# Kernel tuning notes

Hardware: AMD Instinct MI355X
Metric: run time of the kernel (lower is better)

The kernel has to match this reference:

```python
import jax, jax.numpy as jnp
import numpy as np

B, C, H, W, G = 4, 256, 64, 64, 4
K = 9  # 3x3 kernel


def _conv1x1(x, w, b):
    return jnp.einsum('bchw,oc->bohw', x, w) + b[None, :, None, None]


def _deform_conv(V, offset, mask, weight, groups):
    # torchvision modulated deform_conv2d, stride=1, pad=1, dil=1, no bias.
    Bs, Cc, Hh, Ww = V.shape
    Cg = Cc // groups
    # offset layout: [B, og, K, 2(y,x), H, W]
    off = offset.reshape(Bs, groups, K, 2, Hh, Ww)
    ky, kx = jnp.meshgrid(jnp.arange(3), jnp.arange(3), indexing='ij')
    ky = ky.reshape(K).astype(offset.dtype)
    kx = kx.reshape(K).astype(offset.dtype)
    hh = jnp.arange(Hh, dtype=offset.dtype)
    ww = jnp.arange(Ww, dtype=offset.dtype)
    # sampling positions [B, G, K, H, W]
    py = off[:, :, :, 0] + (hh[:, None] - 1.0)[None, None, None] + ky[None, None, :, None, None]
    px = off[:, :, :, 1] + (ww[None, :] - 1.0)[None, None, None] + kx[None, None, :, None, None]
    y0f = jnp.floor(py)
    x0f = jnp.floor(px)
    fy = py - y0f
    fx = px - x0f
    y0 = y0f.astype(jnp.int32)
    x0 = x0f.astype(jnp.int32)
    Vg = V.reshape(Bs, groups, Cg, Hh * Ww)

    def gather(yi, xi, wgt):
        valid = (yi >= 0) & (yi < Hh) & (xi >= 0) & (xi < Ww)
        idx = (jnp.clip(yi, 0, Hh - 1) * Ww + jnp.clip(xi, 0, Ww - 1)).reshape(Bs, groups, 1, K * Hh * Ww)
        vals = jnp.take_along_axis(Vg, jnp.broadcast_to(idx, (Bs, groups, Cg, K * Hh * Ww)), axis=3)
        vals = vals.reshape(Bs, groups, Cg, K, Hh, Ww)
        return vals * (wgt * valid.astype(wgt.dtype))[:, :, None]

    sampled = (gather(y0, x0, (1.0 - fy) * (1.0 - fx))
               + gather(y0, x0 + 1, (1.0 - fy) * fx)
               + gather(y0 + 1, x0, fy * (1.0 - fx))
               + gather(y0 + 1, x0 + 1, fy * fx))  # [B, G, Cg, K, H, W]
    m = mask.reshape(Bs, groups, K, Hh, Ww)
    wk = weight.reshape(groups, Cc // groups, Cg, K)
    out = jnp.einsum('bgikhw,bgkhw,goik->bgohw', sampled, m, wk)
    return out.reshape(Bs, Cc, Hh, Ww)


def setup_inputs() -> dict:
    key = jax.random.key(0)
    ks = jax.random.split(key, 12)
    inp = {
        'rife_feat': jax.random.normal(ks[0], (B, C, H, W), jnp.float32),
        'd0': jax.random.normal(ks[1], (B, C, H, W), jnp.float32),
        'd1': jax.random.normal(ks[2], (B, C, H, W), jnp.float32),
        'wq': jax.random.normal(ks[3], (C, C), jnp.float32) * (1.0 / np.sqrt(C)),
        'bq': jax.random.normal(ks[4], (C,), jnp.float32) * 0.01,
        'wk': jax.random.normal(ks[5], (C, C), jnp.float32) * (1.0 / np.sqrt(C)),
        'bk': jax.random.normal(ks[6], (C,), jnp.float32) * 0.01,
        'wv': jax.random.normal(ks[7], (C, C), jnp.float32) * (1.0 / np.sqrt(C)),
        'bv': jax.random.normal(ks[8], (C,), jnp.float32) * 0.01,
        'w_off': jax.random.normal(ks[9], (27 * G, 2 * C, 3, 3), jnp.float32) * 0.02,
        'b_off': jnp.zeros((27 * G,), jnp.float32),
        'dcn_w': jax.random.normal(ks[10], (C, C // G, 3, 3), jnp.float32) * 0.05,
        'gamma': jnp.ones((1,), jnp.float32),
    }
    return inp


def reference(rife_feat, d0, d1, wq, bq, wk, bk, wv, bv, w_off, b_off, dcn_w, gamma):
    Qs = jnp.concatenate([rife_feat, rife_feat], axis=0)  # [2B, C, H, W]
    Ds = jnp.concatenate([d0, d1], axis=0)
    Q = _conv1x1(Qs, wq, bq)
    Kf = _conv1x1(Ds, wk, bk)
    V = _conv1x1(Ds, wv, bv)
    comb = jnp.concatenate([Q, Kf], axis=1)  # [2B, 2C, H, W]
    out = jax.lax.conv_general_dilated(comb, w_off, (1, 1), [(1, 1), (1, 1)],
                                       dimension_numbers=('NCHW', 'OIHW', 'NCHW'))
    out = out + b_off[None, :, None, None]  # [2B, 27G, H, W]
    n = out.shape[1] // 3
    o1, o2, mlog = out[:, :n], out[:, n:2 * n], out[:, 2 * n:]
    offset = jnp.concatenate([o1, o2], axis=1)  # [2B, 18G, H, W]
    mask = jax.nn.sigmoid(mlog)
    aligned = _deform_conv(V, offset, mask, dcn_w, G)
    a0, a1 = aligned[:B], aligned[B:]
    fused = rife_feat + gamma * (a0 + a1)
    return fused, offset[:B], offset[B:]
```

## Files before the change

kernel.cpp:

```cpp
#include <hip/hip_runtime.h>
#include <math.h>

#define HW   4096
#define CDIM 256

typedef float f32x4  __attribute__((ext_vector_type(4)));
typedef short short8 __attribute__((ext_vector_type(8)));

#define FUSED_SZ (4ULL*256*HW)
#define OFF_SZ   (4ULL*72*HW)

static __device__ __forceinline__ unsigned short f2b(float f) {
    unsigned u = __float_as_uint(f);
    unsigned r = (u + 0x7fffu + ((u >> 16) & 1u)) >> 16;
    return (unsigned short)r;
}
static __device__ __forceinline__ float b2f(short h) {
    return __uint_as_float(((unsigned)(unsigned short)h) << 16);
}
static __device__ __forceinline__ unsigned pk_bf16(float a, float b) {
    unsigned r;
    asm("v_cvt_pk_bf16_f32 %0, %1, %2" : "=v"(r) : "v"(a), "v"(b));
    return r;
}
union U8 { unsigned u[4]; short8 s; };

__global__ __launch_bounds__(256) void prep_all(
    const float* __restrict__ w_off, const float* __restrict__ dcn_w,
    const float* __restrict__ wq, const float* __restrict__ wk,
    const float* __restrict__ wv,
    unsigned short* __restrict__ wT2, unsigned short* __restrict__ dcnwT,
    unsigned short* __restrict__ wqkvT)
{
    const int bid = blockIdx.x;
    if (bid < 2304) {
        int idx = bid * 256 + threadIdx.x;
        int kk  = idx / (128 * 512);
        int rem = idx - kk * 128 * 512;
        int o = rem >> 9;
        int c = rem & 511;
        float v = (o < 108) ? w_off[((size_t)o * 512 + c) * 9 + kk] : 0.f;
        size_t flat = ((size_t)(kk * 16 + (c >> 5)) * 128 + o) * 32 + (c & 31);
        wT2[flat] = f2b(v);
    } else if (bid < 2880) {
        int idx = (bid - 2304) * 256 + threadIdx.x;
        if (idx < 9 * 256 * 64) {
            int k   = idx / (256 * 64);
            int rem = idx - k * 256 * 64;
            int og = rem >> 6;
            int i  = rem & 63;
            int g = og >> 6, ol = og & 63;
            size_t flat = ((size_t)((k * 4 + g) * 2 + (i >> 5)) * 64 + ol) * 32 + (i & 31);
            dcnwT[flat] = f2b(dcn_w[((size_t)og * 64 + i) * 9 + k]);
        }
    } else {
        int idx = (bid - 2880) * 256 + threadIdx.x;
        int o = idx >> 8;
        int c = idx & 255;
        float v = (o < 256) ? wq[(size_t)o * 256 + c]
                : (o < 512) ? wk[(size_t)(o - 256) * 256 + c]
                            : wv[(size_t)(o - 512) * 256 + c];
        wqkvT[idx] = f2b(v);
    }
}

__global__ __launch_bounds__(256) void xprep(
    const float* __restrict__ rife, const float* __restrict__ d0,
    const float* __restrict__ d1, unsigned short* __restrict__ xT)
{
    const int pix0 = blockIdx.x * 64;
    const int img  = blockIdx.y;
    const int t    = threadIdx.x;

    const float* src = (img < 4) ? rife + (size_t)img * CDIM * HW
                     : (img < 8) ? d0 + (size_t)(img - 4) * CDIM * HW
                                 : d1 + (size_t)(img - 8) * CDIM * HW;
    unsigned short* dst = xT + (size_t)img * 4096 * 256;

    __shared__ float tile[64][65];

    for (int c0 = 0; c0 < 256; c0 += 64) {
        #pragma unroll
        for (int r = 0; r < 16; ++r) {
            int idx = t + r * 256;
            int c = idx >> 6, pp = idx & 63;
            tile[c][pp] = src[(size_t)(c0 + c) * HW + pix0 + pp];
        }
        __syncthreads();
        const int pix = t >> 2, cq = t & 3;
        const int cb = cq * 16;
        uint4 p0, p1;
        p0.x = pk_bf16(tile[cb+0][pix],  tile[cb+1][pix]);
        p0.y = pk_bf16(tile[cb+2][pix],  tile[cb+3][pix]);
        p0.z = pk_bf16(tile[cb+4][pix],  tile[cb+5][pix]);
        p0.w = pk_bf16(tile[cb+6][pix],  tile[cb+7][pix]);
        p1.x = pk_bf16(tile[cb+8][pix],  tile[cb+9][pix]);
        p1.y = pk_bf16(tile[cb+10][pix], tile[cb+11][pix]);
        p1.z = pk_bf16(tile[cb+12][pix], tile[cb+13][pix]);
        p1.w = pk_bf16(tile[cb+14][pix], tile[cb+15][pix]);
        unsigned short* p = dst + (size_t)(pix0 + pix) * 256 + c0 + cb;
        *(uint4*)p = p0;
        *(uint4*)(p + 8) = p1;
        __syncthreads();
    }
}

__global__ __launch_bounds__(256) void qkv_mfma(
    const unsigned short* __restrict__ xT,
    const unsigned short* __restrict__ wqkvT,
    const float* __restrict__ bq, const float* __restrict__ bk,
    const float* __restrict__ bv,
    unsigned short* __restrict__ comb_t, unsigned short* __restrict__ vbuf_t)
{
    const int pix0 = blockIdx.x * 64;
    const int type = blockIdx.y;
    const int s    = blockIdx.z;
    const int t    = threadIdx.x;
    const int wvi  = t >> 6;
    const int lane = t & 63;
    const int q    = lane >> 4;
    const int rl   = lane & 15;

    const int img = (type == 0) ? (s & 3) : (4 + s);
    const short8* X = (const short8*)(xT + (size_t)img * 4096 * 256);
    const short8* W = (const short8*)(wqkvT + (size_t)(type * 256 + wvi * 64) * 256);
    const float* bias = (type == 0) ? bq : (type == 1) ? bk : bv;

    f32x4 acc[4][4];
    #pragma unroll
    for (int mf = 0; mf < 4; ++mf)
        #pragma unroll
        for (int nf = 0; nf < 4; ++nf)
            acc[mf][nf] = (f32x4){0.f, 0.f, 0.f, 0.f};

    #pragma unroll
    for (int c8 = 0; c8 < 32; c8 += 4) {
        short8 a[4], b[4];
        #pragma unroll
        for (int mf = 0; mf < 4; ++mf)
            a[mf] = W[(size_t)(mf * 16 + rl) * 32 + c8 + q];
        #pragma unroll
        for (int nf = 0; nf < 4; ++nf)
            b[nf] = X[(size_t)(pix0 + nf * 16 + rl) * 32 + c8 + q];
        #pragma unroll
        for (int mf = 0; mf < 4; ++mf)
            #pragma unroll
            for (int nf = 0; nf < 4; ++nf)
                acc[mf][nf] = __builtin_amdgcn_mfma_f32_16x16x32_bf16(a[mf], b[nf], acc[mf][nf], 0, 0, 0);
    }

    const int CH = (type < 2) ? 512 : 256;
    unsigned short* dst = (type < 2)
        ? comb_t + (size_t)s * 4096 * 512 + type * 256
        : vbuf_t + (size_t)s * 4096 * 256;
    #pragma unroll
    for (int mf = 0; mf < 4; ++mf) {
        const int o_loc = wvi * 64 + mf * 16 + q * 4;
        const float4 bz = *(const float4*)(bias + o_loc);
        #pragma unroll
        for (int nf = 0; nf < 4; ++nf) {
            const int pix = pix0 + nf * 16 + rl;
            uint2 pk;
            pk.x = pk_bf16(acc[mf][nf][0] + bz.x, acc[mf][nf][1] + bz.y);
            pk.y = pk_bf16(acc[mf][nf][2] + bz.z, acc[mf][nf][3] + bz.w);
            *(uint2*)(dst + (size_t)pix * CH + o_loc) = pk;
        }
    }
}

__global__ __launch_bounds__(256) void offconv_mfma(
    const unsigned short* __restrict__ comb_t,
    const unsigned short* __restrict__ wT2,
    const float* __restrict__ b_off,
    float* __restrict__ dout, float* __restrict__ mask_ws)
{
    const int bid = blockIdx.x;
    const int s = bid & 7;
    const int h = bid >> 3;
    const int t = threadIdx.x;
    const int lane = t & 63;
    const int wid  = t >> 6;
    const int q    = lane >> 4;
    const int rl   = lane & 15;

    __shared__ __align__(16) unsigned short tb[2][792 * 8];

    const short8* cbv = (const short8*)comb_t + (size_t)s * 4096 * 64;
    const short8* wv  = (const short8*)wT2;

    const int i1 = t + 256, i2 = t + 512, i3 = t + 768;

    auto sload = [&](int idx, int c8) -> short8 {
        int x = idx >> 2, cq = idx & 3;
        int ky = x / 66, xx = x - ky * 66;
        int hh = h + ky - 1, gx = xx - 1;
        short8 v = {0, 0, 0, 0, 0, 0, 0, 0};
        if (hh >= 0 && hh < 64 && gx >= 0 && gx < 64)
            v = cbv[(size_t)(hh * 64 + gx) * 64 + c8 + cq];
        return v;
    };
    auto swrite = [&](unsigned short* buf, int idx, short8 v) {
        int x = idx >> 2, cq = idx & 3;
        int qs = cq ^ ((x >> 1) & 3);
        *((short8*)buf + x * 4 + qs) = v;
    };

    f32x4 acc[2][4];
    #pragma unroll
    for (int ma = 0; ma < 2; ++ma)
        #pragma unroll
        for (int nf = 0; nf < 4; ++nf)
            acc[ma][nf] = (f32x4){0.f, 0.f, 0.f, 0.f};

    short8 r0 = sload(t, 0), r1 = sload(i1, 0), r2 = sload(i2, 0);
    short8 r3 = {0,0,0,0,0,0,0,0};
    if (i3 < 792) r3 = sload(i3, 0);
    swrite(tb[0], t, r0); swrite(tb[0], i1, r1); swrite(tb[0], i2, r2);
    if (i3 < 792) swrite(tb[0], i3, r3);
    __syncthreads();

    for (int sl = 0; sl < 16; ++sl) {
        const int c8 = sl * 4;
        if (sl < 15) {
            r0 = sload(t, c8 + 4); r1 = sload(i1, c8 + 4); r2 = sload(i2, c8 + 4);
            if (i3 < 792) r3 = sload(i3, c8 + 4);
        }
        short8 a[2][9];
        #pragma unroll
        for (int ma = 0; ma < 2; ++ma) {
            const int o = (wid * 2 + ma) * 16 + rl;
            #pragma unroll
            for (int kk = 0; kk < 9; ++kk)
                a[ma][kk] = wv[((size_t)(kk * 16 + sl) * 128 + o) * 4 + q];
        }
        const unsigned short* bufc = tb[sl & 1];
        #pragma unroll
        for (int kk = 0; kk < 9; ++kk) {
            const int ky = kk / 3, kx = kk % 3;
            #pragma unroll
            for (int nf = 0; nf < 4; ++nf) {
                const int xr = ky * 66 + nf * 16 + rl + kx;
                short8 b = *((const short8*)bufc + xr * 4 + (q ^ ((xr >> 1) & 3)));
                acc[0][nf] = __builtin_amdgcn_mfma_f32_16x16x32_bf16(a[0][kk], b, acc[0][nf], 0, 0, 0);
                acc[1][nf] = __builtin_amdgcn_mfma_f32_16x16x32_bf16(a[1][kk], b, acc[1][nf], 0, 0, 0);
            }
        }
        if (sl < 15) {
            unsigned short* bufn = tb[(sl + 1) & 1];
            swrite(bufn, t, r0); swrite(bufn, i1, r1); swrite(bufn, i2, r2);
            if (i3 < 792) swrite(bufn, i3, r3);
        }
        __syncthreads();
    }

    const size_t obase = FUSED_SZ + (s < 4 ? 0 : OFF_SZ) + (size_t)(s & 3) * 72 * HW + (size_t)h * 64;
    const size_t mbase = (size_t)s * 36 * HW + (size_t)h * 64;
    #pragma unroll
    for (int ma = 0; ma < 2; ++ma) {
        #pragma unroll
        for (int r = 0; r < 4; ++r) {
            const int o = (wid * 2 + ma) * 16 + q * 4 + r;
            if (o >= 108) continue;
            const float bz = b_off[o];
            #pragma unroll
            for (int nf = 0; nf < 4; ++nf) {
                const int w = nf * 16 + rl;
                float v = acc[ma][nf][r] + bz;
                if (o < 72)
                    dout[obase + (size_t)o * HW + w] = v;
                else
                    mask_ws[mbase + (size_t)(o - 72) * HW + w] = 1.f / (1.f + expf(-v));
            }
        }
    }
}

__global__ __launch_bounds__(256) void dcn_fuse_mfma(
    const float* __restrict__ rife, const unsigned short* __restrict__ dcnwT,
    const float* __restrict__ gamma,
    const unsigned short* __restrict__ vbuf_t, const float* __restrict__ mask_ws,
    float* __restrict__ dout)
{
    const int bid = blockIdx.x;
    const int c   = bid & 15;
    const int h   = bid >> 4;
    const int b   = c >> 2;
    const int g   = c & 3;
    const int t    = threadIdx.x;
    const int wv   = t >> 6;
    const int lane = t & 63;
    const int q    = lane >> 4;
    const int rl   = lane & 15;
    const int pix  = wv * 16 + rl;

    const short8* aT = (const short8*)dcnwT;

    f32x4 acc[4];
    #pragma unroll
    for (int ma = 0; ma < 4; ++ma) acc[ma] = (f32x4){0.f, 0.f, 0.f, 0.f};

    const size_t obA = FUSED_SZ + (size_t)b * 72 * HW + (size_t)(g * 18) * HW + (size_t)h * 64 + pix;
    const size_t obB = obA + OFF_SZ;
    const size_t mbA = (size_t)b * 36 * HW + (size_t)(g * 9) * HW + (size_t)h * 64 + pix;
    const size_t mbB = mbA + 4ULL * 36 * HW;

    const unsigned short* VbA = vbuf_t + (size_t)b * 4096 * 256 + g * 64 + q * 8;
    const unsigned short* VbB = VbA + 4ULL * 4096 * 256;

    auto bil = [&](float py, float px, float mv,
                   float& w00, float& w01, float& w10, float& w11,
                   size_t& o00, size_t& o01, size_t& o10, size_t& o11) {
        const float y0f = floorf(py), x0f = floorf(px);
        const float fy = py - y0f, fx = px - x0f;
        const int y0 = (int)y0f, x0 = (int)x0f;
        const bool vy0 = (y0 >= 0) && (y0 < 64);
        const bool vy1 = (y0 >= -1) && (y0 < 63);
        const bool vx0 = (x0 >= 0) && (x0 < 64);
        const bool vx1 = (x0 >= -1) && (x0 < 63);
        w00 = (1.f - fy) * (1.f - fx) * mv * (float)(vy0 && vx0);
        w01 = (1.f - fy) * fx        * mv * (float)(vy0 && vx1);
        w10 = fy * (1.f - fx)        * mv * (float)(vy1 && vx0);
        w11 = fy * fx                * mv * (float)(vy1 && vx1);
        const int yc0 = min(max(y0, 0), 63),     yc1 = min(max(y0 + 1, 0), 63);
        const int xc0 = min(max(x0, 0), 63),     xc1 = min(max(x0 + 1, 0), 63);
        o00 = (size_t)(yc0 * 64 + xc0) * 256;
        o01 = (size_t)(yc0 * 64 + xc1) * 256;
        o10 = (size_t)(yc1 * 64 + xc0) * 256;
        o11 = (size_t)(yc1 * 64 + xc1) * 256;
    };
    auto blend1 = [&](short8 c00, short8 c01, short8 c10, short8 c11,
                      float w00, float w01, float w10, float w11) -> short8 {
        U8 u;
        #pragma unroll
        for (int j = 0; j < 4; ++j) {
            const int ce = 2 * j, co = 2 * j + 1;
            float e0 = w00 * b2f(c00[ce]) + w01 * b2f(c01[ce])
                     + w10 * b2f(c10[ce]) + w11 * b2f(c11[ce]);
            float e1 = w00 * b2f(c00[co]) + w01 * b2f(c01[co])
                     + w10 * b2f(c10[co]) + w11 * b2f(c11[co]);
            u.u[j] = pk_bf16(e0, e1);
        }
        return u.s;
    };

    float cyA = dout[obA], cxA = dout[obA + HW], cmA = mask_ws[mbA];
    float cyB = dout[obB], cxB = dout[obB + HW], cmB = mask_ws[mbB];

    for (int k = 0; k < 9; ++k) {
        const int ky = k / 3, kx = k - ky * 3;

        float wA00, wA01, wA10, wA11, wB00, wB01, wB10, wB11;
        size_t oA00, oA01, oA10, oA11, oB00, oB01, oB10, oB11;
        bil(cyA + (float)(h - 1 + ky), cxA + (float)(pix - 1 + kx), cmA,
            wA00, wA01, wA10, wA11, oA00, oA01, oA10, oA11);
        bil(cyB + (float)(h - 1 + ky), cxB + (float)(pix - 1 + kx), cmB,
            wB00, wB01, wB10, wB11, oB00, oB01, oB10, oB11);

        float nyA = cyA, nxA = cxA, nmA = cmA;
        float nyB = cyB, nxB = cxB, nmB = cmB;
        if (k < 8) {
            nyA = dout[obA + (size_t)((k + 1) * 2) * HW];
            nxA = dout[obA + (size_t)((k + 1) * 2 + 1) * HW];
            nmA = mask_ws[mbA + (size_t)(k + 1) * HW];
            nyB = dout[obB + (size_t)((k + 1) * 2) * HW];
            nxB = dout[obB + (size_t)((k + 1) * 2 + 1) * HW];
            nmB = mask_ws[mbB + (size_t)(k + 1) * HW];
        }

        #pragma unroll
        for (int ks = 0; ks < 2; ++ks) {
            const int co = ks * 32;
            short8 af0 = aT[((size_t)((k * 4 + g) * 2 + ks) * 64 + 0 * 16 + rl) * 4 + q];
            short8 af1 = aT[((size_t)((k * 4 + g) * 2 + ks) * 64 + 1 * 16 + rl) * 4 + q];
            short8 af2 = aT[((size_t)((k * 4 + g) * 2 + ks) * 64 + 2 * 16 + rl) * 4 + q];
            short8 af3 = aT[((size_t)((k * 4 + g) * 2 + ks) * 64 + 3 * 16 + rl) * 4 + q];
            short8 A00 = *(const short8*)(VbA + oA00 + co);
            short8 A01 = *(const short8*)(VbA + oA01 + co);
            short8 A10 = *(const short8*)(VbA + oA10 + co);
            short8 A11 = *(const short8*)(VbA + oA11 + co);
            short8 B00 = *(const short8*)(VbB + oB00 + co);
            short8 B01 = *(const short8*)(VbB + oB01 + co);
            short8 B10 = *(const short8*)(VbB + oB10 + co);
            short8 B11 = *(const short8*)(VbB + oB11 + co);

            short8 bfA = blend1(A00, A01, A10, A11, wA00, wA01, wA10, wA11);
            acc[0] = __builtin_amdgcn_mfma_f32_16x16x32_bf16(af0, bfA, acc[0], 0, 0, 0);
            acc[1] = __builtin_amdgcn_mfma_f32_16x16x32_bf16(af1, bfA, acc[1], 0, 0, 0);
            acc[2] = __builtin_amdgcn_mfma_f32_16x16x32_bf16(af2, bfA, acc[2], 0, 0, 0);
            acc[3] = __builtin_amdgcn_mfma_f32_16x16x32_bf16(af3, bfA, acc[3], 0, 0, 0);
            short8 bfB = blend1(B00, B01, B10, B11, wB00, wB01, wB10, wB11);
            acc[0] = __builtin_amdgcn_mfma_f32_16x16x32_bf16(af0, bfB, acc[0], 0, 0, 0);
            acc[1] = __builtin_amdgcn_mfma_f32_16x16x32_bf16(af1, bfB, acc[1], 0, 0, 0);
            acc[2] = __builtin_amdgcn_mfma_f32_16x16x32_bf16(af2, bfB, acc[2], 0, 0, 0);
            acc[3] = __builtin_amdgcn_mfma_f32_16x16x32_bf16(af3, bfB, acc[3], 0, 0, 0);
        }

        cyA = nyA; cxA = nxA; cmA = nmA;
        cyB = nyB; cxB = nxB; cmB = nmB;
    }

    const float gm = gamma[0];
    #pragma unroll
    for (int ma = 0; ma < 4; ++ma) {
        #pragma unroll
        for (int r = 0; r < 4; ++r) {
            const int o = g * 64 + ma * 16 + q * 4 + r;
            const size_t addr = ((size_t)b * 256 + o) * HW + (size_t)h * 64 + pix;
            dout[addr] = rife[addr] + gm * acc[ma][r];
        }
    }
}

extern "C" void kernel_launch(void* const* d_in, const int* in_sizes, int n_in,
                              void* d_out, int out_size, void* d_ws, size_t ws_size,
                              hipStream_t stream)
{
    const float* rife  = (const float*)d_in[0];
    const float* d0    = (const float*)d_in[1];
    const float* d1    = (const float*)d_in[2];
    const float* wq    = (const float*)d_in[3];
    const float* bq    = (const float*)d_in[4];
    const float* wk    = (const float*)d_in[5];
    const float* bk    = (const float*)d_in[6];
    const float* wv    = (const float*)d_in[7];
    const float* bv    = (const float*)d_in[8];
    const float* w_off = (const float*)d_in[9];
    const float* b_off = (const float*)d_in[10];
    const float* dcnw  = (const float*)d_in[11];
    const float* gamma = (const float*)d_in[12];
    float* out = (float*)d_out;
    char* wsb  = (char*)d_ws;

    unsigned short* comb_t = (unsigned short*)(wsb);
    unsigned short* vbuf_t = (unsigned short*)(wsb + 33554432);
    float*          mws    = (float*)(wsb + 50331648);
    unsigned short* wT2    = (unsigned short*)(wsb + 55050240);
    unsigned short* dcnwT  = (unsigned short*)(wsb + 56229888);
    unsigned short* xT     = (unsigned short*)(wsb + 56524800);
    unsigned short* wqkvT  = (unsigned short*)(wsb + 81690624);

    prep_all<<<3648, 256, 0, stream>>>(w_off, dcnw, wq, wk, wv, wT2, dcnwT, wqkvT);
    xprep<<<dim3(64, 12), 256, 0, stream>>>(rife, d0, d1, xT);
    qkv_mfma<<<dim3(64, 3, 8), 256, 0, stream>>>(xT, wqkvT, bq, bk, bv, comb_t, vbuf_t);
    offconv_mfma<<<512, 256, 0, stream>>>(comb_t, wT2, b_off, out, mws);
    dcn_fuse_mfma<<<1024, 256, 0, stream>>>(rife, dcnwT, gamma, vbuf_t, mws, out);
}
```

Measured before the change: 220.0 us.

## Split DCN A/B halves across two wave groups with LDS reduction

The deformable-conv kernel now launches 512 threads per block. The first four waves process the batch-A (d0) samples and the second four process batch-B (d1), where before each thread handled both serially. Partial accumulators from the B half are reduced through a 16KB shared-memory buffer and a barrier before the fused output write. This doubles wave-level parallelism and halves the per-thread gather latency chain. The cost is the LDS traffic, the sync, and redundant weight-fragment loads in both halves.

```diff
diff --git a/kernel.cpp b/kernel.cpp
--- a/kernel.cpp
+++ b/kernel.cpp
@@ -275,7 +275,7 @@
     }
 }
 
-__global__ __launch_bounds__(256) void dcn_fuse_mfma(
+__global__ __launch_bounds__(512) void dcn_fuse_mfma(
     const float* __restrict__ rife, const unsigned short* __restrict__ dcnwT,
     const float* __restrict__ gamma,
     const unsigned short* __restrict__ vbuf_t, const float* __restrict__ mask_ws,
@@ -287,7 +287,9 @@
     const int b   = c >> 2;
     const int g   = c & 3;
     const int t    = threadIdx.x;
-    const int wv   = t >> 6;
+    const int wave = t >> 6;
+    const int sbi  = wave >> 2;
+    const int wv   = wave & 3;
     const int lane = t & 63;
     const int q    = lane >> 4;
     const int rl   = lane & 15;
@@ -295,17 +297,16 @@
 
     const short8* aT = (const short8*)dcnwT;
 
+    __shared__ __align__(16) float red[256 * 16];
+
     f32x4 acc[4];
     #pragma unroll
     for (int ma = 0; ma < 4; ++ma) acc[ma] = (f32x4){0.f, 0.f, 0.f, 0.f};
 
-    const size_t obA = FUSED_SZ + (size_t)b * 72 * HW + (size_t)(g * 18) * HW + (size_t)h * 64 + pix;
-    const size_t obB = obA + OFF_SZ;
-    const size_t mbA = (size_t)b * 36 * HW + (size_t)(g * 9) * HW + (size_t)h * 64 + pix;
-    const size_t mbB = mbA + 4ULL * 36 * HW;
-
-    const unsigned short* VbA = vbuf_t + (size_t)b * 4096 * 256 + g * 64 + q * 8;
-    const unsigned short* VbB = VbA + 4ULL * 4096 * 256;
+    const size_t ob = FUSED_SZ + (sbi ? OFF_SZ : 0)
+                    + (size_t)b * 72 * HW + (size_t)(g * 18) * HW + (size_t)h * 64 + pix;
+    const size_t mb = (size_t)(sbi * 4 + b) * 36 * HW + (size_t)(g * 9) * HW + (size_t)h * 64 + pix;
+    const unsigned short* Vb = vbuf_t + (size_t)(sbi * 4 + b) * 4096 * 256 + g * 64 + q * 8;
 
     auto bil = [&](float py, float px, float mv,
                    float& w00, float& w01, float& w10, float& w11,
@@ -343,28 +344,21 @@
         return u.s;
     };
 
-    float cyA = dout[obA], cxA = dout[obA + HW], cmA = mask_ws[mbA];
-    float cyB = dout[obB], cxB = dout[obB + HW], cmB = mask_ws[mbB];
+    float cy = dout[ob], cx = dout[ob + HW], cm = mask_ws[mb];
 
     for (int k = 0; k < 9; ++k) {
         const int ky = k / 3, kx = k - ky * 3;
 
-        float wA00, wA01, wA10, wA11, wB00, wB01, wB10, wB11;
-        size_t oA00, oA01, oA10, oA11, oB00, oB01, oB10, oB11;
-        bil(cyA + (float)(h - 1 + ky), cxA + (float)(pix - 1 + kx), cmA,
-            wA00, wA01, wA10, wA11, oA00, oA01, oA10, oA11);
-        bil(cyB + (float)(h - 1 + ky), cxB + (float)(pix - 1 + kx), cmB,
-            wB00, wB01, wB10, wB11, oB00, oB01, oB10, oB11);
-
-        float nyA = cyA, nxA = cxA, nmA = cmA;
-        float nyB = cyB, nxB = cxB, nmB = cmB;
+        float w00, w01, w10, w11;
+        size_t o00, o01, o10, o11;
+        bil(cy + (float)(h - 1 + ky), cx + (float)(pix - 1 + kx), cm,
+            w00, w01, w10, w11, o00, o01, o10, o11);
+
+        float ny = cy, nx = cx, nm = cm;
         if (k < 8) {
-            nyA = dout[obA + (size_t)((k + 1) * 2) * HW];
-            nxA = dout[obA + (size_t)((k + 1) * 2 + 1) * HW];
-            nmA = mask_ws[mbA + (size_t)(k + 1) * HW];
-            nyB = dout[obB + (size_t)((k + 1) * 2) * HW];
-            nxB = dout[obB + (size_t)((k + 1) * 2 + 1) * HW];
-            nmB = mask_ws[mbB + (size_t)(k + 1) * HW];
+            ny = dout[ob + (size_t)((k + 1) * 2) * HW];
+            nx = dout[ob + (size_t)((k + 1) * 2 + 1) * HW];
+            nm = mask_ws[mb + (size_t)(k + 1) * HW];
         }
 
         #pragma unroll
@@ -374,39 +368,40 @@
             short8 af1 = aT[((size_t)((k * 4 + g) * 2 + ks) * 64 + 1 * 16 + rl) * 4 + q];
             short8 af2 = aT[((size_t)((k * 4 + g) * 2 + ks) * 64 + 2 * 16 + rl) * 4 + q];
             short8 af3 = aT[((size_t)((k * 4 + g) * 2 + ks) * 64 + 3 * 16 + rl) * 4 + q];
-            short8 A00 = *(const short8*)(VbA + oA00 + co);
-            short8 A01 = *(const short8*)(VbA + oA01 + co);
-            short8 A10 = *(const short8*)(VbA + oA10 + co);
-            short8 A11 = *(const short8*)(VbA + oA11 + co);
-            short8 B00 = *(const short8*)(VbB + oB00 + co);
-            short8 B01 = *(const short8*)(VbB + oB01 + co);
-            short8 B10 = *(const short8*)(VbB + oB10 + co);
-            short8 B11 = *(const short8*)(VbB + oB11 + co);
-
-            short8 bfA = blend1(A00, A01, A10, A11, wA00, wA01, wA10, wA11);
-            acc[0] = __builtin_amdgcn_mfma_f32_16x16x32_bf16(af0, bfA, acc[0], 0, 0, 0);
-            acc[1] = __builtin_amdgcn_mfma_f32_16x16x32_bf16(af1, bfA, acc[1], 0, 0, 0);
-            acc[2] = __builtin_amdgcn_mfma_f32_16x16x32_bf16(af2, bfA, acc[2], 0, 0, 0);
-            acc[3] = __builtin_amdgcn_mfma_f32_16x16x32_bf16(af3, bfA, acc[3], 0, 0, 0);
-            short8 bfB = blend1(B00, B01, B10, B11, wB00, wB01, wB10, wB11);
-            acc[0] = __builtin_amdgcn_mfma_f32_16x16x32_bf16(af0, bfB, acc[0], 0, 0, 0);
-            acc[1] = __builtin_amdgcn_mfma_f32_16x16x32_bf16(af1, bfB, acc[1], 0, 0, 0);
-            acc[2] = __builtin_amdgcn_mfma_f32_16x16x32_bf16(af2, bfB, acc[2], 0, 0, 0);
-            acc[3] = __builtin_amdgcn_mfma_f32_16x16x32_bf16(af3, bfB, acc[3], 0, 0, 0);
-        }
-
-        cyA = nyA; cxA = nxA; cmA = nmA;
-        cyB = nyB; cxB = nxB; cmB = nmB;
-    }
-
-    const float gm = gamma[0];
-    #pragma unroll
-    for (int ma = 0; ma < 4; ++ma) {
-        #pragma unroll
-        for (int r = 0; r < 4; ++r) {
-            const int o = g * 64 + ma * 16 + q * 4 + r;
-            const size_t addr = ((size_t)b * 256 + o) * HW + (size_t)h * 64 + pix;
-            dout[addr] = rife[addr] + gm * acc[ma][r];
+            short8 C00 = *(const short8*)(Vb + o00 + co);
+            short8 C01 = *(const short8*)(Vb + o01 + co);
+            short8 C10 = *(const short8*)(Vb + o10 + co);
+            short8 C11 = *(const short8*)(Vb + o11 + co);
+
+            short8 bf = blend1(C00, C01, C10, C11, w00, w01, w10, w11);
+            acc[0] = __builtin_amdgcn_mfma_f32_16x16x32_bf16(af0, bf, acc[0], 0, 0, 0);
+            acc[1] = __builtin_amdgcn_mfma_f32_16x16x32_bf16(af1, bf, acc[1], 0, 0, 0);
+            acc[2] = __builtin_amdgcn_mfma_f32_16x16x32_bf16(af2, bf, acc[2], 0, 0, 0);
+            acc[3] = __builtin_amdgcn_mfma_f32_16x16x32_bf16(af3, bf, acc[3], 0, 0, 0);
+        }
+
+        cy = ny; cx = nx; cm = nm;
+    }
+
+    if (sbi == 1) {
+        float* dst = &red[(t - 256) * 16];
+        #pragma unroll
+        for (int ma = 0; ma < 4; ++ma)
+            *(f32x4*)(dst + ma * 4) = acc[ma];
+    }
+    __syncthreads();
+    if (sbi == 0) {
+        const float* src = &red[t * 16];
+        const float gm = gamma[0];
+        #pragma unroll
+        for (int ma = 0; ma < 4; ++ma) {
+            f32x4 other = *(const f32x4*)(src + ma * 4);
+            #pragma unroll
+            for (int r = 0; r < 4; ++r) {
+                const int o = g * 64 + ma * 16 + q * 4 + r;
+                const size_t addr = ((size_t)b * 256 + o) * HW + (size_t)h * 64 + pix;
+                dout[addr] = rife[addr] + gm * (acc[ma][r] + other[r]);
+            }
         }
     }
 }
@@ -443,5 +438,5 @@
     xprep<<<dim3(64, 12), 256, 0, stream>>>(rife, d0, d1, xT);
     qkv_mfma<<<dim3(64, 3, 8), 256, 0, stream>>>(xT, wqkvT, bq, bk, bv, comb_t, vbuf_t);
     offconv_mfma<<<512, 256, 0, stream>>>(comb_t, wT2, b_off, out, mws);
-    dcn_fuse_mfma<<<1024, 256, 0, stream>>>(rife, dcnwT, gamma, vbuf_t, mws, out);
-}
+    dcn_fuse_mfma<<<1024, 512, 0, stream>>>(rife, dcnwT, gamma, vbuf_t, mws, out);
+}
```

Result: slower. 235.9 us (+7.2%).
